# Optimization experiments

Hardware: AMD Instinct MI355X
Metric: run time of the kernel (lower is better)

Reference implementation:

```python
import jax, jax.numpy as jnp
import numpy as np

D_MODEL = 2048
NUM_HEADS = 16
KV_HEADS = 4
HEAD_DIM = D_MODEL // NUM_HEADS  # 128
SEQ = 4096
BATCH = 1
ROPE_THETA = 10000.0


def _rope_cache(T, dim, base, dtype):
    inv_freq = 1.0 / (base ** (jnp.arange(0, dim, 2, dtype=jnp.float32) / dim))
    t = jnp.arange(T, dtype=jnp.float32)
    freqs = jnp.outer(t, inv_freq)                      # (T, dim/2)
    emb = jnp.concatenate([freqs, freqs], axis=-1)      # (T, dim)
    return jnp.cos(emb).astype(dtype), jnp.sin(emb).astype(dtype)


def _rotate_half(x):
    d = x.shape[-1] // 2
    return jnp.concatenate([-x[..., d:], x[..., :d]], axis=-1)


def _apply_rope(q, k, cos, sin):
    # q: (B,T,Hq,D), k: (B,T,Hkv,D); cos/sin: (T,D) broadcast over heads
    c = cos[None, :, None, :]
    s = sin[None, :, None, :]
    q = q * c + _rotate_half(q) * s
    k = k * c + _rotate_half(k) * s
    return q, k


def setup_inputs() -> dict:
    key = jax.random.key(0)
    ks = jax.random.split(key, 6)
    sc = 1.0 / np.sqrt(D_MODEL)
    kv_out = KV_HEADS * HEAD_DIM
    return {
        "x": jax.random.normal(ks[0], (BATCH, SEQ, D_MODEL), dtype=jnp.float32),
        "Wq": jax.random.normal(ks[1], (D_MODEL, D_MODEL), dtype=jnp.float32) * sc,
        "Wk": jax.random.normal(ks[2], (D_MODEL, kv_out), dtype=jnp.float32) * sc,
        "Wv": jax.random.normal(ks[3], (D_MODEL, kv_out), dtype=jnp.float32) * sc,
        "Wo": jax.random.normal(ks[4], (D_MODEL, D_MODEL), dtype=jnp.float32) * sc,
        "bo": jax.random.normal(ks[5], (D_MODEL,), dtype=jnp.float32) * 0.01,
    }


def reference(x, Wq, Wk, Wv, Wo, bo):
    B, T, _ = x.shape
    q = (x @ Wq).reshape(B, T, NUM_HEADS, HEAD_DIM)
    k = (x @ Wk).reshape(B, T, KV_HEADS, HEAD_DIM)
    v = (x @ Wv).reshape(B, T, KV_HEADS, HEAD_DIM)

    cos, sin = _rope_cache(T, HEAD_DIM, ROPE_THETA, x.dtype)
    q, k = _apply_rope(q, k, cos, sin)

    reps = NUM_HEADS // KV_HEADS
    k = jnp.repeat(k, reps, axis=2)  # repeat_interleave on head dim
    v = jnp.repeat(v, reps, axis=2)

    # (B,H,T,D)
    q = q.transpose(0, 2, 1, 3)
    k = k.transpose(0, 2, 1, 3)
    v = v.transpose(0, 2, 1, 3)

    scores = jnp.einsum("bhqd,bhkd->bhqk", q, k)
    causal = jnp.triu(jnp.ones((T, T), dtype=bool), k=1)
    scores = jnp.where(causal[None, None], -jnp.inf, scores)
    attn = jax.nn.softmax(scores / jnp.sqrt(jnp.asarray(HEAD_DIM, x.dtype)), axis=-1)

    ctx = jnp.einsum("bhqk,bhkd->bhqd", attn, v)
    ctx = ctx.transpose(0, 2, 1, 3).reshape(B, T, D_MODEL)
    return ctx @ Wo + bo
```

## Files before the change

### kernel.cpp

```cpp
#include <hip/hip_runtime.h>
#include <cstdint>
#include <cstddef>

#define SEQ 4096
#define DM  2048
#define NH  16
#define KVH 4
#define HD  128

typedef short bf16_t;
typedef __attribute__((ext_vector_type(8))) short bf16x8;
typedef __attribute__((ext_vector_type(4))) float f32x4;

__device__ __forceinline__ bf16_t f2b(float f) {
  unsigned u = __builtin_bit_cast(unsigned, f);
  u += 0x7fffu + ((u >> 16) & 1u);
  return (bf16_t)(u >> 16);
}
__device__ __forceinline__ float b2f(bf16_t s) {
  unsigned u = ((unsigned)(unsigned short)s) << 16;
  return __builtin_bit_cast(float, u);
}

__device__ __forceinline__ void gload_lds16(const void* gsrc, void* ldst) {
  __builtin_amdgcn_global_load_lds(
      (__attribute__((address_space(1))) void*)gsrc,
      (__attribute__((address_space(3))) void*)ldst, 16, 0, 0);
}

__global__ void cast_x_bf16(const float* __restrict__ x, bf16_t* __restrict__ xb, int n4) {
  int i = blockIdx.x * 256 + threadIdx.x;
  if (i >= n4) return;
  float4 v = ((const float4*)x)[i];
  union { bf16_t h[4]; unsigned long long u; } o;
  o.h[0] = f2b(v.x); o.h[1] = f2b(v.y); o.h[2] = f2b(v.z); o.h[3] = f2b(v.w);
  ((unsigned long long*)xb)[i] = o.u;
}

__global__ void transpose_cast_w(const float* __restrict__ W, bf16_t* __restrict__ Wt,
                                 int K, int N) {
  __shared__ float tile[32][33];
  int k0 = blockIdx.y * 32, n0 = blockIdx.x * 32;
  int tx = threadIdx.x, ty = threadIdx.y;
#pragma unroll
  for (int dy = 0; dy < 32; dy += 8)
    tile[ty + dy][tx] = W[(size_t)(k0 + ty + dy) * N + n0 + tx];
  __syncthreads();
#pragma unroll
  for (int dy = 0; dy < 32; dy += 8)
    Wt[(size_t)(n0 + ty + dy) * K + k0 + tx] = f2b(tile[tx][ty + dy]);
}

__global__ void rope_tab(float* __restrict__ ct, float* __restrict__ st) {
  int i = blockIdx.x * 256 + threadIdx.x;
  if (i >= SEQ * 64) return;
  int t = i >> 6, j = i & 63;
  float invf = expf(-(float)j * (9.210340371976184f / 64.0f));
  float ang = (float)t * invf;
  ct[i] = cosf(ang);
  st[i] = sinf(ang);
}

__global__ void rope_apply(bf16_t* __restrict__ Qb, bf16_t* __restrict__ KVb,
                           const float* __restrict__ ct, const float* __restrict__ st) {
  int i = blockIdx.x * 256 + threadIdx.x;
  const int qtot = SEQ * NH * 64;
  const int tot = qtot + SEQ * KVH * 64;
  if (i >= tot) return;
  bf16_t* base; int t, j;
  if (i < qtot) {
    t = i >> 10; int rem = i & 1023; int hh = rem >> 6; j = rem & 63;
    base = Qb + (size_t)t * DM + hh * HD;
  } else {
    int i2 = i - qtot;
    t = i2 >> 8; int rem = i2 & 255; int hh = rem >> 6; j = rem & 63;
    base = KVb + (size_t)t * 1024 + hh * HD;
  }
  float c = ct[t * 64 + j], s = st[t * 64 + j];
  float x0 = b2f(base[j]);
  float x1 = b2f(base[j + 64]);
  base[j]      = f2b(x0 * c - x1 * s);
  base[j + 64] = f2b(x1 * c + x0 * s);
}

__global__ void transpose_v(const bf16_t* __restrict__ KVb, bf16_t* __restrict__ Vt) {
  __shared__ bf16_t tile[32][33];
  int t0 = blockIdx.y * 32, d0 = blockIdx.x * 32;
  int tx = threadIdx.x, ty = threadIdx.y;
#pragma unroll
  for (int dy = 0; dy < 32; dy += 8)
    tile[ty + dy][tx] = KVb[(size_t)(t0 + ty + dy) * 1024 + 512 + d0 + tx];
  __syncthreads();
#pragma unroll
  for (int dy = 0; dy < 32; dy += 8)
    Vt[(size_t)(d0 + ty + dy) * SEQ + t0 + tx] = tile[tx][ty + dy];
}

template <int BIAS>
__global__ __launch_bounds__(256, 2)
void gemm_bt(const bf16_t* __restrict__ A, const bf16_t* __restrict__ Bt,
             void* __restrict__ Cout, const float* __restrict__ bias,
             int M, int N, int K) {
  __shared__ __align__(16) bf16_t ldsA[128 * 64];
  __shared__ __align__(16) bf16_t ldsB[128 * 64];
  const int t = threadIdx.x;
  const int w = t >> 6, l = t & 63;
  const int lg = l >> 4, lr = l & 15;
  const int bm = blockIdx.y, bn = blockIdx.x;
  const int wr = (w >> 1) * 64, wc = (w & 1) * 64;

  f32x4 acc[4][4] = {};

  for (int k0 = 0; k0 < K; k0 += 64) {
    __syncthreads();
#pragma unroll
    for (int i = 0; i < 4; ++i) {
      int idx = i * 256 + t;
      int row = idx >> 3;
      int ch  = (idx & 7) ^ (row & 7);
      gload_lds16(A  + (size_t)(bm * 128 + row) * K + k0 + ch * 8, &ldsA[idx * 8]);
      gload_lds16(Bt + (size_t)(bn * 128 + row) * K + k0 + ch * 8, &ldsB[idx * 8]);
    }
    __syncthreads();
#pragma unroll
    for (int kk = 0; kk < 2; ++kk) {
      bf16x8 af[4], bfr[4];
#pragma unroll
      for (int m = 0; m < 4; ++m) {
        int row = wr + m * 16 + lr;
        int ch = (kk * 4 + lg) ^ (row & 7);
        af[m] = *(const bf16x8*)&ldsA[row * 64 + ch * 8];
      }
#pragma unroll
      for (int n = 0; n < 4; ++n) {
        int row = wc + n * 16 + lr;
        int ch = (kk * 4 + lg) ^ (row & 7);
        bfr[n] = *(const bf16x8*)&ldsB[row * 64 + ch * 8];
      }
#pragma unroll
      for (int m = 0; m < 4; ++m)
#pragma unroll
        for (int n = 0; n < 4; ++n)
          acc[m][n] = __builtin_amdgcn_mfma_f32_16x16x32_bf16(af[m], bfr[n], acc[m][n], 0, 0, 0);
    }
  }

  const int row0 = bm * 128 + wr + lg * 4;
  const int col0 = bn * 128 + wc + lr;
  if (BIAS) {
    float* C = (float*)Cout;
#pragma unroll
    for (int n = 0; n < 4; ++n) {
      int col = col0 + n * 16;
      float b = bias[col];
#pragma unroll
      for (int m = 0; m < 4; ++m)
#pragma unroll
        for (int r = 0; r < 4; ++r)
          C[(size_t)(row0 + m * 16 + r) * N + col] = acc[m][n][r] + b;
    }
  } else {
    bf16_t* C = (bf16_t*)Cout;
#pragma unroll
    for (int m = 0; m < 4; ++m)
#pragma unroll
      for (int n = 0; n < 4; ++n) {
        int col = col0 + n * 16;
#pragma unroll
        for (int r = 0; r < 4; ++r)
          C[(size_t)(row0 + m * 16 + r) * N + col] = f2b(acc[m][n][r]);
      }
  }
}

__global__ __launch_bounds__(256, 2)
void attn_fwd(const bf16_t* __restrict__ Qb, const bf16_t* __restrict__ KVb,
              const bf16_t* __restrict__ Vt, bf16_t* __restrict__ ctx) {
  __shared__ __align__(16) bf16_t kt[2][64 * 128];
  __shared__ __align__(16) bf16_t vts[2][128 * 64];
  __shared__ __align__(16) bf16_t plds[4][2][16 * 64];

  const int t = threadIdx.x;
  const int w = t >> 6, l = t & 63;
  const int lg = l >> 4, lr = l & 15;
  const int h = blockIdx.y, g = h >> 2;
  const int b = blockIdx.x;
  const int qt0 = b, qt1 = 63 - b;

  bf16x8 qf[2][4];
#pragma unroll
  for (int kk = 0; kk < 4; ++kk) {
    qf[0][kk] = *(const bf16x8*)&Qb[(size_t)(qt0 * 64 + w * 16 + lr) * DM + h * HD + kk * 32 + lg * 8];
    qf[1][kk] = *(const bf16x8*)&Qb[(size_t)(qt1 * 64 + w * 16 + lr) * DM + h * HD + kk * 32 + lg * 8];
  }

  f32x4 acc[2][9] = {};
  float m_run[2] = {-1e30f, -1e30f};

  bf16x8 ones;
#pragma unroll
  for (int i = 0; i < 8; ++i) ones[i] = (short)0x3F80;

  const float sl2e = 0.08838834764831845f * 1.4426950408889634f;
  const int swz = (lr & 7) << 1;

  const bf16_t* ksrc = KVb + g * 128;
  const bf16_t* vsrc = Vt + (size_t)(g * 128) * SEQ;
  auto stage = [&](int buf, int kvt) {
#pragma unroll
    for (int i = 0; i < 4; ++i) {
      int idx = i * 256 + t;
      int row = idx >> 4;
      int ch = (idx & 15) ^ (row & 7);
      gload_lds16(ksrc + (size_t)(kvt * 64 + row) * 1024 + ch * 8, &kt[buf][idx * 8]);
    }
#pragma unroll
    for (int i = 0; i < 4; ++i) {
      int idx = i * 256 + t;
      int row = idx >> 3;
      int ch = (idx & 7) ^ (row & 7);
      gload_lds16(vsrc + (size_t)row * SEQ + kvt * 64 + ch * 8, &vts[buf][idx * 8]);
    }
  };

  const int nkv = qt1 + 1;
  stage(0, 0);

  for (int kv = 0; kv < nkv; ++kv) {
    const int cur = kv & 1;
    const int kv0 = kv * 64;
    __syncthreads();
    if (kv + 1 < nkv) stage(cur ^ 1, kv + 1);

    const bool act0 = kv <= qt0;

    f32x4 s[2][4];
#pragma unroll
    for (int m = 0; m < 2; ++m)
#pragma unroll
      for (int n = 0; n < 4; ++n) s[m][n] = f32x4{0.f, 0.f, 0.f, 0.f};

    __builtin_amdgcn_s_setprio(1);
#pragma unroll
    for (int n = 0; n < 4; ++n) {
      int row = n * 16 + lr;
#pragma unroll
      for (int kk = 0; kk < 4; ++kk) {
        int ch = (kk * 4 + lg) ^ (row & 7);
        bf16x8 kf = *(const bf16x8*)&kt[cur][row * 128 + ch * 8];
        if (act0) s[0][n] = __builtin_amdgcn_mfma_f32_16x16x32_bf16(kf, qf[0][kk], s[0][n], 0, 0, 0);
        s[1][n] = __builtin_amdgcn_mfma_f32_16x16x32_bf16(kf, qf[1][kk], s[1][n], 0, 0, 0);
      }
    }
    __builtin_amdgcn_s_setprio(0);

#pragma unroll
    for (int m = 0; m < 2; ++m) {
      if (m == 0 && !act0) continue;
      const int qtm = (m == 0) ? qt0 : qt1;
      const int qrow = qtm * 64 + w * 16 + lr;

      if (kv == qtm) {
#pragma unroll
        for (int n = 0; n < 4; ++n)
#pragma unroll
          for (int r = 0; r < 4; ++r) {
            int key = kv0 + n * 16 + lg * 4 + r;
            if (key > qrow) s[m][n][r] = -1e30f;
          }
      }

      float pm0 = fmaxf(fmaxf(s[m][0][0], s[m][0][1]), fmaxf(s[m][0][2], s[m][0][3]));
      float pm1 = fmaxf(fmaxf(s[m][1][0], s[m][1][1]), fmaxf(s[m][1][2], s[m][1][3]));
      float pm2 = fmaxf(fmaxf(s[m][2][0], s[m][2][1]), fmaxf(s[m][2][2], s[m][2][3]));
      float pm3 = fmaxf(fmaxf(s[m][3][0], s[m][3][1]), fmaxf(s[m][3][2], s[m][3][3]));
      float pm = fmaxf(fmaxf(pm0, pm1), fmaxf(pm2, pm3));
      pm = fmaxf(pm, __shfl_xor(pm, 16, 64));
      pm = fmaxf(pm, __shfl_xor(pm, 32, 64));

      if (__any((int)(pm > m_run[m] + 60.f))) {
        float mn = fmaxf(m_run[m], pm);
        float a_s = exp2f((m_run[m] - mn) * sl2e);
        m_run[m] = mn;
        float alpha[4];
#pragma unroll
        for (int r = 0; r < 4; ++r)
          alpha[r] = __shfl(a_s, (l & 48) | (lg * 4 + r), 64);
#pragma unroll
        for (int nd = 0; nd < 9; ++nd)
#pragma unroll
          for (int r = 0; r < 4; ++r)
            acc[m][nd][r] *= alpha[r];
      }

#pragma unroll
      for (int n = 0; n < 4; ++n) {
        union { bf16_t h[4]; unsigned long long u; } pk;
#pragma unroll
        for (int r = 0; r < 4; ++r)
          pk.h[r] = f2b(exp2f((s[m][n][r] - m_run[m]) * sl2e));
        int gr = (n * 4 + lg) ^ swz;
        *(unsigned long long*)&plds[w][m][lr * 64 + gr * 4] = pk.u;
      }
    }

#pragma unroll
    for (int kk2 = 0; kk2 < 2; ++kk2) {
      int gg = ((kk2 * 8 + lg * 2) ^ swz);
      bf16x8 pf0 = *(const bf16x8*)&plds[w][0][lr * 64 + gg * 4];
      bf16x8 pf1 = *(const bf16x8*)&plds[w][1][lr * 64 + gg * 4];
      __builtin_amdgcn_s_setprio(1);
#pragma unroll
      for (int nd = 0; nd < 8; ++nd) {
        int vrow = nd * 16 + lr;
        int vch = (kk2 * 4 + lg) ^ (vrow & 7);
        bf16x8 vf = *(const bf16x8*)&vts[cur][vrow * 64 + vch * 8];
        if (act0) acc[0][nd] = __builtin_amdgcn_mfma_f32_16x16x32_bf16(pf0, vf, acc[0][nd], 0, 0, 0);
        acc[1][nd] = __builtin_amdgcn_mfma_f32_16x16x32_bf16(pf1, vf, acc[1][nd], 0, 0, 0);
      }
      if (act0) acc[0][8] = __builtin_amdgcn_mfma_f32_16x16x32_bf16(pf0, ones, acc[0][8], 0, 0, 0);
      acc[1][8] = __builtin_amdgcn_mfma_f32_16x16x32_bf16(pf1, ones, acc[1][8], 0, 0, 0);
      __builtin_amdgcn_s_setprio(0);
    }
  }

#pragma unroll
  for (int m = 0; m < 2; ++m) {
    const int qtm = (m == 0) ? qt0 : qt1;
#pragma unroll
    for (int r = 0; r < 4; ++r) {
      float rl = 1.0f / acc[m][8][r];
      int qrow = qtm * 64 + w * 16 + lg * 4 + r;
#pragma unroll
      for (int nd = 0; nd < 8; ++nd) {
        int col = h * HD + nd * 16 + lr;
        ctx[(size_t)qrow * DM + col] = f2b(acc[m][nd][r] * rl);
      }
    }
  }
}

extern "C" void kernel_launch(void* const* d_in, const int* in_sizes, int n_in,
                              void* d_out, int out_size, void* d_ws, size_t ws_size,
                              hipStream_t stream) {
  const float* x  = (const float*)d_in[0];
  const float* Wq = (const float*)d_in[1];
  const float* Wk = (const float*)d_in[2];
  const float* Wv = (const float*)d_in[3];
  const float* Wo = (const float*)d_in[4];
  const float* bo = (const float*)d_in[5];
  float* out = (float*)d_out;

  char* p = (char*)d_ws;
  bf16_t* xb   = (bf16_t*)p;
  bf16_t* ctx  = xb;
  p += (size_t)SEQ * DM * 2;
  bf16_t* Wqt  = (bf16_t*)p; p += (size_t)DM * DM * 2;
  bf16_t* Wkvt = (bf16_t*)p; p += (size_t)1024 * DM * 2;
  bf16_t* Wot  = (bf16_t*)p; p += (size_t)DM * DM * 2;
  bf16_t* Qb   = (bf16_t*)p; p += (size_t)SEQ * DM * 2;
  bf16_t* KVb  = (bf16_t*)p; p += (size_t)SEQ * 1024 * 2;
  bf16_t* Vt   = (bf16_t*)p; p += (size_t)512 * SEQ * 2;
  float*  ctab = (float*)p;  p += (size_t)SEQ * 64 * 4;
  float*  stab = (float*)p;  p += (size_t)SEQ * 64 * 4;

  cast_x_bf16<<<(SEQ * DM / 4 + 255) / 256, 256, 0, stream>>>(x, xb, SEQ * DM / 4);
  transpose_cast_w<<<dim3(DM / 32, DM / 32), dim3(32, 8), 0, stream>>>(Wq, Wqt, DM, DM);
  transpose_cast_w<<<dim3(512 / 32, DM / 32), dim3(32, 8), 0, stream>>>(Wk, Wkvt, DM, 512);
  transpose_cast_w<<<dim3(512 / 32, DM / 32), dim3(32, 8), 0, stream>>>(Wv, Wkvt + (size_t)512 * DM, DM, 512);
  transpose_cast_w<<<dim3(DM / 32, DM / 32), dim3(32, 8), 0, stream>>>(Wo, Wot, DM, DM);
  rope_tab<<<(SEQ * 64 + 255) / 256, 256, 0, stream>>>(ctab, stab);

  gemm_bt<0><<<dim3(DM / 128, SEQ / 128), 256, 0, stream>>>(xb, Wqt, Qb, nullptr, SEQ, DM, DM);
  gemm_bt<0><<<dim3(1024 / 128, SEQ / 128), 256, 0, stream>>>(xb, Wkvt, KVb, nullptr, SEQ, 1024, DM);

  rope_apply<<<(SEQ * (NH + KVH) * 64 + 255) / 256, 256, 0, stream>>>(Qb, KVb, ctab, stab);
  transpose_v<<<dim3(512 / 32, SEQ / 32), dim3(32, 8), 0, stream>>>(KVb, Vt);

  attn_fwd<<<dim3(32, NH), 256, 0, stream>>>(Qb, KVb, Vt, ctx);

  gemm_bt<1><<<dim3(DM / 128, SEQ / 128), 256, 0, stream>>>(ctx, Wot, out, bo, SEQ, DM, DM);
}
```

Before: 299.9 us.

## Keep softmax probabilities in registers and fold the softmax scale into Q

The P matrix is no longer round-tripped through LDS. Instead, V is stored in a permuted key order so that the MFMA output layout of S can be packed straight into the A-operand fragment with v_cvt_pk_bf16_f32. The 1/sqrt(d)*log2e scale is folded into Q during the RoPE pass, which removes a per-element multiply, and the rescale threshold becomes 8 in the scaled domain. The softmax for the two query tiles is interleaved with the PV MFMAs to overlap them, at some extra register cost.

```diff
diff --git a/kernel.cpp b/kernel.cpp
--- a/kernel.cpp
+++ b/kernel.cpp
@@ -7,10 +7,12 @@
 #define NH  16
 #define KVH 4
 #define HD  128
+#define QSCALE (0.08838834764831845f * 1.4426950408889634f)
 
 typedef short bf16_t;
 typedef __attribute__((ext_vector_type(8))) short bf16x8;
 typedef __attribute__((ext_vector_type(4))) float f32x4;
+typedef __attribute__((ext_vector_type(4))) unsigned uint32x4;
 
 __device__ __forceinline__ bf16_t f2b(float f) {
   unsigned u = __builtin_bit_cast(unsigned, f);
@@ -20,6 +22,11 @@
 __device__ __forceinline__ float b2f(bf16_t s) {
   unsigned u = ((unsigned)(unsigned short)s) << 16;
   return __builtin_bit_cast(float, u);
+}
+__device__ __forceinline__ unsigned cvtpk(float lo, float hi) {
+  unsigned r;
+  asm("v_cvt_pk_bf16_f32 %0, %1, %2" : "=v"(r) : "v"(lo), "v"(hi));
+  return r;
 }
 
 __device__ __forceinline__ void gload_lds16(const void* gsrc, void* ldst) {
@@ -67,20 +74,22 @@
   const int qtot = SEQ * NH * 64;
   const int tot = qtot + SEQ * KVH * 64;
   if (i >= tot) return;
-  bf16_t* base; int t, j;
+  bf16_t* base; int t, j; float scl;
   if (i < qtot) {
     t = i >> 10; int rem = i & 1023; int hh = rem >> 6; j = rem & 63;
     base = Qb + (size_t)t * DM + hh * HD;
+    scl = QSCALE;
   } else {
     int i2 = i - qtot;
     t = i2 >> 8; int rem = i2 & 255; int hh = rem >> 6; j = rem & 63;
     base = KVb + (size_t)t * 1024 + hh * HD;
+    scl = 1.0f;
   }
   float c = ct[t * 64 + j], s = st[t * 64 + j];
   float x0 = b2f(base[j]);
   float x1 = b2f(base[j + 64]);
-  base[j]      = f2b(x0 * c - x1 * s);
-  base[j + 64] = f2b(x1 * c + x0 * s);
+  base[j]      = f2b((x0 * c - x1 * s) * scl);
+  base[j + 64] = f2b((x1 * c + x0 * s) * scl);
 }
 
 __global__ void transpose_v(const bf16_t* __restrict__ KVb, bf16_t* __restrict__ Vt) {
@@ -91,9 +100,11 @@
   for (int dy = 0; dy < 32; dy += 8)
     tile[ty + dy][tx] = KVb[(size_t)(t0 + ty + dy) * 1024 + 512 + d0 + tx];
   __syncthreads();
+  int tt = t0 + tx;
+  int j = (tt & ~63) | (tt & 32) | ((tt & 12) << 1) | ((tt & 16) >> 2) | (tt & 3);
 #pragma unroll
   for (int dy = 0; dy < 32; dy += 8)
-    Vt[(size_t)(d0 + ty + dy) * SEQ + t0 + tx] = tile[tx][ty + dy];
+    Vt[(size_t)(d0 + ty + dy) * SEQ + j] = tile[tx][ty + dy];
 }
 
 template <int BIAS>
@@ -178,7 +189,6 @@
               const bf16_t* __restrict__ Vt, bf16_t* __restrict__ ctx) {
   __shared__ __align__(16) bf16_t kt[2][64 * 128];
   __shared__ __align__(16) bf16_t vts[2][128 * 64];
-  __shared__ __align__(16) bf16_t plds[4][2][16 * 64];
 
   const int t = threadIdx.x;
   const int w = t >> 6, l = t & 63;
@@ -201,9 +211,6 @@
 #pragma unroll
   for (int i = 0; i < 8; ++i) ones[i] = (short)0x3F80;
 
-  const float sl2e = 0.08838834764831845f * 1.4426950408889634f;
-  const int swz = (lr & 7) << 1;
-
   const bf16_t* ksrc = KVb + g * 128;
   const bf16_t* vsrc = Vt + (size_t)(g * 128) * SEQ;
   auto stage = [&](int buf, int kvt) {
@@ -254,34 +261,31 @@
     }
     __builtin_amdgcn_s_setprio(0);
 
-#pragma unroll
-    for (int m = 0; m < 2; ++m) {
-      if (m == 0 && !act0) continue;
-      const int qtm = (m == 0) ? qt0 : qt1;
+    auto softmax = [&](f32x4 (&sv)[4], float& mr, f32x4 (&am)[9], int qtm,
+                       bf16x8 (&pf)[2]) {
       const int qrow = qtm * 64 + w * 16 + lr;
-
       if (kv == qtm) {
 #pragma unroll
         for (int n = 0; n < 4; ++n)
 #pragma unroll
           for (int r = 0; r < 4; ++r) {
             int key = kv0 + n * 16 + lg * 4 + r;
-            if (key > qrow) s[m][n][r] = -1e30f;
+            if (key > qrow) sv[n][r] = -1e30f;
           }
       }
-
-      float pm0 = fmaxf(fmaxf(s[m][0][0], s[m][0][1]), fmaxf(s[m][0][2], s[m][0][3]));
-      float pm1 = fmaxf(fmaxf(s[m][1][0], s[m][1][1]), fmaxf(s[m][1][2], s[m][1][3]));
-      float pm2 = fmaxf(fmaxf(s[m][2][0], s[m][2][1]), fmaxf(s[m][2][2], s[m][2][3]));
-      float pm3 = fmaxf(fmaxf(s[m][3][0], s[m][3][1]), fmaxf(s[m][3][2], s[m][3][3]));
-      float pm = fmaxf(fmaxf(pm0, pm1), fmaxf(pm2, pm3));
+      float pm = sv[0][0];
+#pragma unroll
+      for (int n = 0; n < 4; ++n)
+#pragma unroll
+        for (int r = 0; r < 4; ++r)
+          pm = fmaxf(pm, sv[n][r]);
       pm = fmaxf(pm, __shfl_xor(pm, 16, 64));
       pm = fmaxf(pm, __shfl_xor(pm, 32, 64));
 
-      if (__any((int)(pm > m_run[m] + 60.f))) {
-        float mn = fmaxf(m_run[m], pm);
-        float a_s = exp2f((m_run[m] - mn) * sl2e);
-        m_run[m] = mn;
+      if (__any((int)(pm > mr + 8.f))) {
+        float mn = fmaxf(mr, pm);
+        float a_s = exp2f(mr - mn);
+        mr = mn;
         float alpha[4];
 #pragma unroll
         for (int r = 0; r < 4; ++r)
@@ -290,38 +294,47 @@
         for (int nd = 0; nd < 9; ++nd)
 #pragma unroll
           for (int r = 0; r < 4; ++r)
-            acc[m][nd][r] *= alpha[r];
-      }
-
+            am[nd][r] *= alpha[r];
+      }
+
+      unsigned u[8];
 #pragma unroll
       for (int n = 0; n < 4; ++n) {
-        union { bf16_t h[4]; unsigned long long u; } pk;
-#pragma unroll
-        for (int r = 0; r < 4; ++r)
-          pk.h[r] = f2b(exp2f((s[m][n][r] - m_run[m]) * sl2e));
-        int gr = (n * 4 + lg) ^ swz;
-        *(unsigned long long*)&plds[w][m][lr * 64 + gr * 4] = pk.u;
-      }
-    }
-
-#pragma unroll
-    for (int kk2 = 0; kk2 < 2; ++kk2) {
-      int gg = ((kk2 * 8 + lg * 2) ^ swz);
-      bf16x8 pf0 = *(const bf16x8*)&plds[w][0][lr * 64 + gg * 4];
-      bf16x8 pf1 = *(const bf16x8*)&plds[w][1][lr * 64 + gg * 4];
-      __builtin_amdgcn_s_setprio(1);
+        u[2 * n]     = cvtpk(exp2f(sv[n][0] - mr), exp2f(sv[n][1] - mr));
+        u[2 * n + 1] = cvtpk(exp2f(sv[n][2] - mr), exp2f(sv[n][3] - mr));
+      }
+      pf[0] = __builtin_bit_cast(bf16x8, (uint32x4){u[0], u[1], u[2], u[3]});
+      pf[1] = __builtin_bit_cast(bf16x8, (uint32x4){u[4], u[5], u[6], u[7]});
+    };
+
+    auto loadvf = [&](bf16x8 (&vf)[8], int kk2) {
 #pragma unroll
       for (int nd = 0; nd < 8; ++nd) {
         int vrow = nd * 16 + lr;
-        int vch = (kk2 * 4 + lg) ^ (vrow & 7);
-        bf16x8 vf = *(const bf16x8*)&vts[cur][vrow * 64 + vch * 8];
-        if (act0) acc[0][nd] = __builtin_amdgcn_mfma_f32_16x16x32_bf16(pf0, vf, acc[0][nd], 0, 0, 0);
-        acc[1][nd] = __builtin_amdgcn_mfma_f32_16x16x32_bf16(pf1, vf, acc[1][nd], 0, 0, 0);
-      }
-      if (act0) acc[0][8] = __builtin_amdgcn_mfma_f32_16x16x32_bf16(pf0, ones, acc[0][8], 0, 0, 0);
-      acc[1][8] = __builtin_amdgcn_mfma_f32_16x16x32_bf16(pf1, ones, acc[1][8], 0, 0, 0);
+        int ch = (kk2 * 4 + lg) ^ (lr & 7);
+        vf[nd] = *(const bf16x8*)&vts[cur][vrow * 64 + ch * 8];
+      }
+    };
+    auto pv = [&](const bf16x8 (&vf)[8], const bf16x8& pfk, f32x4 (&am)[9]) {
+      __builtin_amdgcn_s_setprio(1);
+#pragma unroll
+      for (int nd = 0; nd < 8; ++nd)
+        am[nd] = __builtin_amdgcn_mfma_f32_16x16x32_bf16(pfk, vf[nd], am[nd], 0, 0, 0);
+      am[8] = __builtin_amdgcn_mfma_f32_16x16x32_bf16(pfk, ones, am[8], 0, 0, 0);
       __builtin_amdgcn_s_setprio(0);
-    }
+    };
+
+    bf16x8 pf0[2], pf1[2];
+    if (act0) softmax(s[0], m_run[0], acc[0], qt0, pf0);
+    bf16x8 vfa[8];
+    loadvf(vfa, 0);
+    if (act0) pv(vfa, pf0[0], acc[0]);
+    softmax(s[1], m_run[1], acc[1], qt1, pf1);
+    pv(vfa, pf1[0], acc[1]);
+    bf16x8 vfb[8];
+    loadvf(vfb, 1);
+    if (act0) pv(vfb, pf0[1], acc[0]);
+    pv(vfb, pf1[1], acc[1]);
   }
 
 #pragma unroll
```

Measured after the change: 281.3 us. 1.07x faster.
